# Kernel tuning notes

Measured on AMD Instinct MI355X. Metric: run time of the kernel, lower is better.

## Reference

```python
import jax, jax.numpy as jnp
import numpy as np

N, V, E = 65536, 2048, 1024
TEMPERATURE = 0.5
EPS = 1e-10
LOG_PARAM_Q = -2.995732273553991


def _l2_normalize(x, axis):
    # matches torch F.normalize(p=2): x / max(||x||, 1e-12)
    n = jnp.sqrt(jnp.sum(x * x, axis=axis, keepdims=True))
    return x / jnp.maximum(n, 1e-12)


def setup_inputs() -> dict:
    key = jax.random.key(0)
    k1, k2, k3 = jax.random.split(key, 3)
    z = jax.random.normal(k1, (N, E), dtype=jnp.float32)
    emb_weight = jax.random.normal(k2, (V, E), dtype=jnp.float32)
    U = jax.random.uniform(k3, (N, V), dtype=jnp.float32)
    return {"z": z, "emb_weight": emb_weight, "U": U}


def reference(z, emb_weight, U):
    kappa_q = jnp.exp(jnp.float32(LOG_PARAM_Q)) + jnp.float32(1.0)
    zn = _l2_normalize(z, axis=1)              # [N, E]
    emb = _l2_normalize(emb_weight, axis=1)    # [V, E]
    # logit = -distances = kappa_q * z @ emb.T
    logit = kappa_q * jnp.matmul(zn, emb.T)    # [N, V]
    # gumbel-softmax sample (training branch)
    g = -jnp.log(-jnp.log(U + EPS) + EPS)
    tokens = jax.nn.softmax((logit + g) / TEMPERATURE, axis=-1)  # [N, V]
    z_q = jnp.matmul(tokens, emb)              # [N, E]
    return (tokens, z_q)
```

## Files before the change

kernel.cpp:

```cpp
#include <hip/hip_runtime.h>
#include <hip/hip_bf16.h>
#include <stdint.h>

typedef short bf16x8 __attribute__((ext_vector_type(8)));
typedef float floatx4 __attribute__((ext_vector_type(4)));

#define N_ROWS 65536
#define V_DIM 2048
#define E_DIM 1024

__device__ __forceinline__ short f2bf(float x) {
  union { float f; uint32_t u; } c; c.f = x;
  uint32_t r = (c.u + 0x7FFFu + ((c.u >> 16) & 1u)) >> 16;
  return (short)(uint16_t)r;
}
__device__ __forceinline__ float bf16f(short b) {
  union { uint32_t u; float f; } c; c.u = ((uint32_t)(uint16_t)b) << 16;
  return c.f;
}

__device__ __forceinline__ float wave_sum(float v) {
#pragma unroll
  for (int o = 32; o > 0; o >>= 1) v += __shfl_xor(v, o);
  return v;
}
__device__ __forceinline__ float wave_max(float v) {
#pragma unroll
  for (int o = 32; o > 0; o >>= 1) v = fmaxf(v, __shfl_xor(v, o));
  return v;
}

__device__ __forceinline__ void gll16(const short* g, short* l) {
  __builtin_amdgcn_global_load_lds(
      (const __attribute__((address_space(1))) void*)g,
      (__attribute__((address_space(3))) void*)l, 16, 0, 0);
}

#define FRAG(base, R, c) \
  (*(const bf16x8*)((const char*)(base) + ((R) << 7) + (((((c) >> 3) ^ ((R) & 7))) << 4)))

__global__ __launch_bounds__(256) void k_norm_emb(const float* __restrict__ W,
                                                  short* __restrict__ embn,
                                                  short* __restrict__ embnT) {
  const int v = blockIdx.x;
  const int t = threadIdx.x;
  const int w = t >> 6, l = t & 63;
  const float4 val = *(const float4*)&W[(size_t)v * E_DIM + t * 4];
  float ss = val.x * val.x + val.y * val.y + val.z * val.z + val.w * val.w;
  ss = wave_sum(ss);
  __shared__ float red[4];
  if (l == 0) red[w] = ss;
  __syncthreads();
  ss = red[0] + red[1] + red[2] + red[3];
  const float inv = 1.0f / fmaxf(sqrtf(ss), 1e-12f);
  short4 o;
  o.x = f2bf(val.x * inv);
  o.y = f2bf(val.y * inv);
  o.z = f2bf(val.z * inv);
  o.w = f2bf(val.w * inv);
  *(short4*)&embn[(size_t)v * E_DIM + t * 4] = o;
  embnT[(size_t)(t * 4 + 0) * V_DIM + v] = o.x;
  embnT[(size_t)(t * 4 + 1) * V_DIM + v] = o.y;
  embnT[(size_t)(t * 4 + 2) * V_DIM + v] = o.z;
  embnT[(size_t)(t * 4 + 3) * V_DIM + v] = o.w;
}

__global__ __launch_bounds__(256) void k_norm_z(const float* __restrict__ Z,
                                                short* __restrict__ zn) {
  const int w = threadIdx.x >> 6, l = threadIdx.x & 63;
  const int row = blockIdx.x * 4 + w;
  const float* zr = Z + (size_t)row * E_DIM;
  float4 v[4];
  float ss = 0.f;
#pragma unroll
  for (int i = 0; i < 4; ++i) {
    v[i] = *(const float4*)&zr[(i * 64 + l) * 4];
    ss += v[i].x * v[i].x + v[i].y * v[i].y + v[i].z * v[i].z + v[i].w * v[i].w;
  }
  ss = wave_sum(ss);
  const float SCALE = 2.0f * (expf(-2.995732273553991f) + 1.0f);
  const float inv = SCALE / fmaxf(sqrtf(ss), 1e-12f);
  short* zo = zn + (size_t)row * E_DIM;
#pragma unroll
  for (int i = 0; i < 4; ++i) {
    short4 o;
    o.x = f2bf(v[i].x * inv);
    o.y = f2bf(v[i].y * inv);
    o.z = f2bf(v[i].z * inv);
    o.w = f2bf(v[i].w * inv);
    *(short4*)&zo[(i * 64 + l) * 4] = o;
  }
}

template <int KDIM, int NBX, int EPI>
__global__ __launch_bounds__(512, 2) void k_gemm8(
    const short* __restrict__ A, const short* __restrict__ B,
    const float* __restrict__ U, short* __restrict__ Pb,
    float* __restrict__ partials, const float* __restrict__ invsum,
    float* __restrict__ C, int cpx) {
  __shared__ __align__(16) short Sm[65536];
  const int NT = KDIM / 32;
  const int tid = threadIdx.x;
  const int wv = tid >> 6, lane = tid & 63;
  const int lr = lane & 15, lh = lane >> 4;
  const int wr = wv >> 2, wc = wv & 3;
  const int d = blockIdx.x;
  const int L = (d & 7) * cpx + (d >> 3);
  const int by = L / NBX, bx = L % NBX;
  const int m0 = by * 256, n0 = bx * 256;
  const int sg = (((lane & 3) ^ ((lane >> 2) & 3) ^ ((lane >> 4) & 3)) << 3);
  const int srow = wv * 16 + (lane >> 2);
  const short* gA = A + (size_t)(m0 + srow) * KDIM + sg;
  const short* gB = B + (size_t)(n0 + srow) * KDIM + sg;
  const int fslot = lh ^ ((lr ^ (lr >> 2)) & 3);
  const int aoff = wr * 8192 + lr * 64 + fslot * 16;
  const int boff = wc * 4096 + lr * 64 + fslot * 16;

#pragma unroll
  for (int t = 0; t < 2; ++t) {
#pragma unroll
    for (int q = 0; q < 2; ++q) {
      gll16(gA + (size_t)(q * 128) * KDIM + t * 32, Sm + t * 8192 + q * 4096 + wv * 512);
      gll16(gB + (size_t)(q * 128) * KDIM + t * 32, Sm + 32768 + t * 8192 + q * 4096 + wv * 512);
    }
  }
  asm volatile("s_waitcnt vmcnt(4)" ::: "memory");
  __builtin_amdgcn_s_barrier();
  __builtin_amdgcn_sched_barrier(0);

  floatx4 acc[8][4] = {};

#define DO_TILE(KT, STAGE, VMN)                                                     \
  {                                                                                 \
    const int cb_ = (KT) & 3;                                                       \
    const char* Ab_ = (const char*)Sm + cb_ * 16384;                                \
    const char* Bb_ = (const char*)Sm + 65536 + cb_ * 16384;                        \
    short* An_ = Sm + (((KT) + 2) & 3) * 8192;                                      \
    short* Bn_ = Sm + 32768 + (((KT) + 2) & 3) * 8192;                              \
    const size_t kc_ = (size_t)((KT) + 2) * 32;                                     \
    bf16x8 bfr[4], af[4];                                                           \
     \
    _Pragma("unroll")                                                               \
    for (int n = 0; n < 4; ++n) bfr[n] = *(const bf16x8*)(Bb_ + boff + n * 1024);   \
    _Pragma("unroll")                                                               \
    for (int i = 0; i < 4; ++i) af[i] = *(const bf16x8*)(Ab_ + aoff + i * 1024);    \
    if (STAGE) {                                                                    \
      gll16(gA + kc_, An_ + wv * 512);                                              \
      gll16(gA + (size_t)128 * KDIM + kc_, An_ + 4096 + wv * 512);                  \
    }                                                                               \
    __builtin_amdgcn_s_barrier();                                                   \
    asm volatile("s_waitcnt lgkmcnt(0)" ::: "memory");                              \
    __builtin_amdgcn_sched_barrier(0);                                              \
    __builtin_amdgcn_s_setprio(1);                                                  \
    _Pragma("unroll")                                                               \
    for (int i = 0; i < 4; ++i) {                                                   \
      _Pragma("unroll")                                                             \
      for (int n = 0; n < 4; ++n)                                                   \
        acc[i][n] =                                                                 \
            __builtin_amdgcn_mfma_f32_16x16x32_bf16(af[i], bfr[n], acc[i][n], 0, 0, 0); \
    }                                                                               \
    __builtin_amdgcn_s_setprio(0);                                                  \
    __builtin_amdgcn_s_barrier();                                                   \
     \
    _Pragma("unroll")                                                               \
    for (int i = 0; i < 4; ++i)                                                     \
      af[i] = *(const bf16x8*)(Ab_ + aoff + 4096 + i * 1024);                       \
    if (STAGE) {                                                                    \
      gll16(gB + kc_, Bn_ + wv * 512);                                              \
      gll16(gB + (size_t)128 * KDIM + kc_, Bn_ + 4096 + wv * 512);                  \
    }                                                                               \
    __builtin_amdgcn_s_barrier();                                                   \
    asm volatile("s_waitcnt lgkmcnt(0)" ::: "memory");                              \
    __builtin_amdgcn_sched_barrier(0);                                              \
    __builtin_amdgcn_s_setprio(1);                                                  \
    _Pragma("unroll")                                                               \
    for (int i = 0; i < 4; ++i) {                                                   \
      _Pragma("unroll")                                                             \
      for (int n = 0; n < 4; ++n)                                                   \
        acc[4 + i][n] =                                                             \
            __builtin_amdgcn_mfma_f32_16x16x32_bf16(af[i], bfr[n], acc[4 + i][n], 0, 0, 0); \
    }                                                                               \
    __builtin_amdgcn_s_setprio(0);                                                  \
    asm volatile("s_waitcnt vmcnt(" #VMN ")" ::: "memory");                         \
    __builtin_amdgcn_s_barrier();                                                   \
    __builtin_amdgcn_sched_barrier(0);                                              \
  }

  for (int kt = 0; kt < NT - 2; ++kt) DO_TILE(kt, 1, 4);
  DO_TILE(NT - 2, 0, 0);
  DO_TILE(NT - 1, 0, 0);
#undef DO_TILE

  const int gr0 = m0 + wr * 128 + lh * 4;
  const int gc0 = n0 + wc * 64 + lr;
  if (EPI == 0) {
    float rs[8][4] = {};
#pragma unroll
    for (int m = 0; m < 8; ++m)
#pragma unroll
      for (int n = 0; n < 4; ++n) {
        const int col = gc0 + n * 16;
#pragma unroll
        for (int j = 0; j < 4; ++j) {
          const int row = gr0 + m * 16 + j;
          const size_t idx = (size_t)row * V_DIM + col;
          const float u = U[idx];
          const float e = __expf(acc[m][n][j] - 2.f * __logf(-__logf(u + 1e-10f) + 1e-10f));
          const short eb = f2bf(e);
          Pb[idx] = eb;
          rs[m][j] += bf16f(eb);
        }
      }
#pragma unroll
    for (int m = 0; m < 8; ++m)
#pragma unroll
      for (int j = 0; j < 4; ++j) {
        float s = rs[m][j];
        s += __shfl_xor(s, 1); s += __shfl_xor(s, 2);
        s += __shfl_xor(s, 4); s += __shfl_xor(s, 8);
        if (lr == 0)
          partials[(size_t)(gr0 + m * 16 + j) * 32 + bx * 4 + wc] = s;
      }
  } else {
#pragma unroll
    for (int m = 0; m < 8; ++m)
#pragma unroll
      for (int j = 0; j < 4; ++j) {
        const int row = gr0 + m * 16 + j;
        const float s = invsum[row];
#pragma unroll
        for (int n = 0; n < 4; ++n)
          C[(size_t)row * E_DIM + gc0 + n * 16] = acc[m][n][j] * s;
      }
  }
}

__global__ __launch_bounds__(256) void k_rowsum_inv(const float* __restrict__ partials,
                                                    float* __restrict__ invsum) {
  const int r = blockIdx.x * 256 + threadIdx.x;
  const float4* p = (const float4*)&partials[(size_t)r * 32];
  float s = 0.f;
#pragma unroll
  for (int i = 0; i < 8; ++i) { float4 v = p[i]; s += v.x + v.y + v.z + v.w; }
  invsum[r] = 1.f / s;
}

__global__ __launch_bounds__(256) void k_token_norm(const short* __restrict__ Pb,
                                                    const float* __restrict__ invsum,
                                                    float* __restrict__ tokens) {
  const size_t stride = (size_t)gridDim.x * 256 * 8;
  for (size_t i = ((size_t)blockIdx.x * 256 + threadIdx.x) * 8;
       i < (size_t)N_ROWS * V_DIM; i += stride) {
    const float s = invsum[i >> 11];
    const bf16x8 v = *(const bf16x8*)&Pb[i];
    float4 o0, o1;
    o0.x = bf16f(v[0]) * s; o0.y = bf16f(v[1]) * s;
    o0.z = bf16f(v[2]) * s; o0.w = bf16f(v[3]) * s;
    o1.x = bf16f(v[4]) * s; o1.y = bf16f(v[5]) * s;
    o1.z = bf16f(v[6]) * s; o1.w = bf16f(v[7]) * s;
    *(float4*)&tokens[i] = o0;
    *(float4*)&tokens[i + 4] = o1;
  }
}

__global__ __launch_bounds__(256) void k_gemm_nt(const short* __restrict__ A,
                                                 const short* __restrict__ B,
                                                 float* __restrict__ C,
                                                 int lda, int ldb, int ldc, int K) {
  __shared__ __align__(16) short As[128][64];
  __shared__ __align__(16) short Bs[128][64];
  const int t = threadIdx.x;
  const int w = t >> 6, l = t & 63;
  const int lr = l & 15, lh = l >> 4;
  const int m0 = blockIdx.y * 128, n0 = blockIdx.x * 128;
  const int wm = (w >> 1) * 64, wn = (w & 1) * 64;
  floatx4 acc[4][4] = {};
  for (int k0 = 0; k0 < K; k0 += 64) {
    __syncthreads();
#pragma unroll
    for (int i = 0; i < 4; ++i) {
      const int c = i * 256 + t;
      const int r = c >> 3, c8 = (c & 7) * 8;
      *(bf16x8*)&As[r][c8] = *(const bf16x8*)&A[(size_t)(m0 + r) * lda + k0 + c8];
      *(bf16x8*)&Bs[r][c8] = *(const bf16x8*)&B[(size_t)(n0 + r) * ldb + k0 + c8];
    }
    __syncthreads();
#pragma unroll
    for (int kk = 0; kk < 64; kk += 32) {
      bf16x8 af[4], bfr[4];
#pragma unroll
      for (int m = 0; m < 4; ++m) af[m] = *(const bf16x8*)&As[wm + m * 16 + lr][kk + lh * 8];
#pragma unroll
      for (int n = 0; n < 4; ++n) bfr[n] = *(const bf16x8*)&Bs[wn + n * 16 + lr][kk + lh * 8];
#pragma unroll
      for (int m = 0; m < 4; ++m)
#pragma unroll
        for (int n = 0; n < 4; ++n)
          acc[m][n] = __builtin_amdgcn_mfma_f32_16x16x32_bf16(af[m], bfr[n], acc[m][n], 0, 0, 0);
    }
  }
#pragma unroll
  for (int m = 0; m < 4; ++m)
#pragma unroll
    for (int n = 0; n < 4; ++n) {
      const int col = n0 + wn + n * 16 + lr;
#pragma unroll
      for (int j = 0; j < 4; ++j)
        C[(size_t)(m0 + wm + m * 16 + lh * 4 + j) * ldc + col] = acc[m][n][j];
    }
}

__global__ __launch_bounds__(256) void k_gemm_nt_f32a(const float* __restrict__ A,
                                                      const short* __restrict__ B,
                                                      float* __restrict__ C,
                                                      int lda, int ldb, int ldc, int K) {
  __shared__ __align__(16) short As[128][64];
  __shared__ __align__(16) short Bs[128][64];
  const int t = threadIdx.x;
  const int w = t >> 6, l = t & 63;
  const int lr = l & 15, lh = l >> 4;
  const int m0 = blockIdx.y * 128, n0 = blockIdx.x * 128;
  const int wm = (w >> 1) * 64, wn = (w & 1) * 64;
  floatx4 acc[4][4] = {};
  for (int k0 = 0; k0 < K; k0 += 64) {
    __syncthreads();
#pragma unroll
    for (int i = 0; i < 4; ++i) {
      const int c = i * 256 + t;
      const int r = c >> 3, c8 = (c & 7) * 8;
      const float4 a0 = *(const float4*)&A[(size_t)(m0 + r) * lda + k0 + c8];
      const float4 a1 = *(const float4*)&A[(size_t)(m0 + r) * lda + k0 + c8 + 4];
      bf16x8 va;
      va[0] = f2bf(a0.x); va[1] = f2bf(a0.y); va[2] = f2bf(a0.z); va[3] = f2bf(a0.w);
      va[4] = f2bf(a1.x); va[5] = f2bf(a1.y); va[6] = f2bf(a1.z); va[7] = f2bf(a1.w);
      *(bf16x8*)&As[r][c8] = va;
      *(bf16x8*)&Bs[r][c8] = *(const bf16x8*)&B[(size_t)(n0 + r) * ldb + k0 + c8];
    }
    __syncthreads();
#pragma unroll
    for (int kk = 0; kk < 64; kk += 32) {
      bf16x8 af[4], bfr[4];
#pragma unroll
      for (int m = 0; m < 4; ++m) af[m] = *(const bf16x8*)&As[wm + m * 16 + lr][kk + lh * 8];
#pragma unroll
      for (int n = 0; n < 4; ++n) bfr[n] = *(const bf16x8*)&Bs[wn + n * 16 + lr][kk + lh * 8];
#pragma unroll
      for (int m = 0; m < 4; ++m)
#pragma unroll
        for (int n = 0; n < 4; ++n)
          acc[m][n] = __builtin_amdgcn_mfma_f32_16x16x32_bf16(af[m], bfr[n], acc[m][n], 0, 0, 0);
    }
  }
#pragma unroll
  for (int m = 0; m < 4; ++m)
#pragma unroll
    for (int n = 0; n < 4; ++n) {
      const int col = n0 + wn + n * 16 + lr;
#pragma unroll
      for (int j = 0; j < 4; ++j)
        C[(size_t)(m0 + wm + m * 16 + lh * 4 + j) * ldc + col] = acc[m][n][j];
    }
}

__global__ __launch_bounds__(256) void k_gumbel_softmax(float* __restrict__ S,
                                                        const float* __restrict__ U) {
  const int t = threadIdx.x;
  const int w = t >> 6, l = t & 63;
  const size_t base = (size_t)blockIdx.x * V_DIM + t * 8;
  const float4 s0 = *(const float4*)&S[base];
  const float4 s1 = *(const float4*)&S[base + 4];
  const float4 u0 = *(const float4*)&U[base];
  const float4 u1 = *(const float4*)&U[base + 4];
  float x[8];
  x[0] = s0.x - 2.f * __logf(-__logf(u0.x + 1e-10f) + 1e-10f);
  x[1] = s0.y - 2.f * __logf(-__logf(u0.y + 1e-10f) + 1e-10f);
  x[2] = s0.z - 2.f * __logf(-__logf(u0.z + 1e-10f) + 1e-10f);
  x[3] = s0.w - 2.f * __logf(-__logf(u0.w + 1e-10f) + 1e-10f);
  x[4] = s1.x - 2.f * __logf(-__logf(u1.x + 1e-10f) + 1e-10f);
  x[5] = s1.y - 2.f * __logf(-__logf(u1.y + 1e-10f) + 1e-10f);
  x[6] = s1.z - 2.f * __logf(-__logf(u1.z + 1e-10f) + 1e-10f);
  x[7] = s1.w - 2.f * __logf(-__logf(u1.w + 1e-10f) + 1e-10f);
  float lm = x[0];
#pragma unroll
  for (int i = 1; i < 8; ++i) lm = fmaxf(lm, x[i]);
  lm = wave_max(lm);
  __shared__ float redA[4], redB[4];
  if (l == 0) redA[w] = lm;
  __syncthreads();
  const float m = fmaxf(fmaxf(redA[0], redA[1]), fmaxf(redA[2], redA[3]));
  float p[8];
  float ls = 0.f;
#pragma unroll
  for (int i = 0; i < 8; ++i) { p[i] = __expf(x[i] - m); ls += p[i]; }
  ls = wave_sum(ls);
  if (l == 0) redB[w] = ls;
  __syncthreads();
  const float inv = 1.0f / (redB[0] + redB[1] + redB[2] + redB[3]);
  float4 o0 = make_float4(p[0] * inv, p[1] * inv, p[2] * inv, p[3] * inv);
  float4 o1 = make_float4(p[4] * inv, p[5] * inv, p[6] * inv, p[7] * inv);
  *(float4*)&S[base] = o0;
  *(float4*)&S[base + 4] = o1;
}

extern "C" void kernel_launch(void* const* d_in, const int* in_sizes, int n_in,
                              void* d_out, int out_size, void* d_ws, size_t ws_size,
                              hipStream_t stream) {
  const float* z = (const float*)d_in[0];
  const float* W = (const float*)d_in[1];
  const float* U = (const float*)d_in[2];
  float* tokens = (float*)d_out;
  float* zq = tokens + (size_t)N_ROWS * V_DIM;
  short* zn = (short*)zq;

  short* embn = (short*)d_ws;
  short* embnT = embn + (size_t)V_DIM * E_DIM;

  const size_t NEED = (size_t)V_DIM * E_DIM * 2 * 2
                    + (size_t)N_ROWS * 32 * 4
                    + (size_t)N_ROWS * 4
                    + (size_t)N_ROWS * V_DIM * 2;

  k_norm_emb<<<V_DIM, 256, 0, stream>>>(W, embn, embnT);
  k_norm_z<<<N_ROWS / 4, 256, 0, stream>>>(z, zn);

  if (ws_size >= NEED) {
    float* partials = (float*)(embnT + (size_t)V_DIM * E_DIM);
    float* invsum = partials + (size_t)N_ROWS * 32;
    short* Pb = (short*)(invsum + N_ROWS);
    k_gemm8<E_DIM, 8, 0><<<2048, 512, 0, stream>>>(
        zn, embn, U, Pb, partials, nullptr, nullptr, 2048 / 8);
    k_rowsum_inv<<<N_ROWS / 256, 256, 0, stream>>>(partials, invsum);
    k_token_norm<<<2048, 256, 0, stream>>>(Pb, invsum, tokens);
    k_gemm8<V_DIM, 4, 1><<<1024, 512, 0, stream>>>(
        Pb, embnT, nullptr, nullptr, nullptr, invsum, zq, 1024 / 8);
  } else {
    k_gemm_nt<<<dim3(V_DIM / 128, N_ROWS / 128), 256, 0, stream>>>(
        zn, embn, tokens, E_DIM, E_DIM, V_DIM, E_DIM);
    k_gumbel_softmax<<<N_ROWS, 256, 0, stream>>>(tokens, U);
    k_gemm_nt_f32a<<<dim3(E_DIM / 128, N_ROWS / 128), 256, 0, stream>>>(
        tokens, embnT, zq, V_DIM, V_DIM, E_DIM, V_DIM);
  }
}
```

Measured before the change: 992.7 us.

## Fuse token normalization into second GEMM epilogue and prefetch U in first

Removes the separate token-normalization kernel. Each block of the second GEMM (tokens @ emb) now also re-reads its 256-row by 512-column slice of the bf16 probabilities, scales it by the inverse row sum and writes fp32 tokens. The block mapping of that GEMM changes so adjacent blocks share column tiles, which keeps the Pb rows hot in cache. In the first GEMM the U loads are issued in groups ahead of the exp/log work to hide global latency, at the cost of many more live registers.

```diff
diff --git a/kernel.cpp b/kernel.cpp
--- a/kernel.cpp
+++ b/kernel.cpp
@@ -97,7 +97,7 @@
     const short* __restrict__ A, const short* __restrict__ B,
     const float* __restrict__ U, short* __restrict__ Pb,
     float* __restrict__ partials, const float* __restrict__ invsum,
-    float* __restrict__ C, int cpx) {
+    float* __restrict__ C, float* __restrict__ tokens, int cpx) {
   __shared__ __align__(16) short Sm[65536];
   const int NT = KDIM / 32;
   const int tid = threadIdx.x;
@@ -106,7 +106,8 @@
   const int wr = wv >> 2, wc = wv & 3;
   const int d = blockIdx.x;
   const int L = (d & 7) * cpx + (d >> 3);
-  const int by = L / NBX, bx = L % NBX;
+  const int by = (EPI == 0) ? (L / NBX) : (L & 255);
+  const int bx = (EPI == 0) ? (L % NBX) : (L >> 8);
   const int m0 = by * 256, n0 = bx * 256;
   const int sg = (((lane & 3) ^ ((lane >> 2) & 3) ^ ((lane >> 4) & 3)) << 3);
   const int srow = wv * 16 + (lane >> 2);
@@ -194,23 +195,50 @@
   const int gr0 = m0 + wr * 128 + lh * 4;
   const int gc0 = n0 + wc * 64 + lr;
   if (EPI == 0) {
+    const float* Ug = U + (size_t)gr0 * V_DIM + gc0;
     float rs[8][4] = {};
-#pragma unroll
-    for (int m = 0; m < 8; ++m)
-#pragma unroll
-      for (int n = 0; n < 4; ++n) {
-        const int col = gc0 + n * 16;
-#pragma unroll
-        for (int j = 0; j < 4; ++j) {
-          const int row = gr0 + m * 16 + j;
-          const size_t idx = (size_t)row * V_DIM + col;
-          const float u = U[idx];
-          const float e = __expf(acc[m][n][j] - 2.f * __logf(-__logf(u + 1e-10f) + 1e-10f));
-          const short eb = f2bf(e);
-          Pb[idx] = eb;
-          rs[m][j] += bf16f(eb);
-        }
-      }
+    float u01[32], u23[32], u45[32], u67[32];
+#define UPREF(arr, P)                                                               \
+    {                                                                               \
+      _Pragma("unroll")                                                             \
+      for (int mm = 0; mm < 2; ++mm)                                                \
+        _Pragma("unroll")                                                           \
+        for (int n = 0; n < 4; ++n)                                                 \
+          _Pragma("unroll")                                                         \
+          for (int j = 0; j < 4; ++j)                                               \
+            arr[mm * 16 + n * 4 + j] =                                              \
+                Ug[(size_t)(((2 * (P) + mm) * 16 + j)) * V_DIM + n * 16];           \
+    }
+#define EPI_PAIR(P, arr)                                                            \
+    _Pragma("unroll")                                                               \
+    for (int mm = 0; mm < 2; ++mm) {                                                \
+      const int m = 2 * (P) + mm;                                                   \
+      _Pragma("unroll")                                                             \
+      for (int n = 0; n < 4; ++n) {                                                 \
+        const int col = gc0 + n * 16;                                               \
+        _Pragma("unroll")                                                           \
+        for (int j = 0; j < 4; ++j) {                                               \
+          const int row = gr0 + m * 16 + j;                                         \
+          const size_t idx = (size_t)row * V_DIM + col;                             \
+          const float u = arr[mm * 16 + n * 4 + j];                                 \
+          const float e = __expf(acc[m][n][j] -                                     \
+                                 2.f * __logf(-__logf(u + 1e-10f) + 1e-10f));       \
+          const short eb = f2bf(e);                                                 \
+          Pb[idx] = eb;                                                             \
+          rs[m][j] += bf16f(eb);                                                    \
+        }                                                                           \
+      }                                                                             \
+    }
+    UPREF(u01, 0);
+    UPREF(u23, 1);
+    UPREF(u45, 2);
+    EPI_PAIR(0, u01);
+    UPREF(u67, 3);
+    EPI_PAIR(1, u23);
+    EPI_PAIR(2, u45);
+    EPI_PAIR(3, u67);
+#undef UPREF
+#undef EPI_PAIR
 #pragma unroll
     for (int m = 0; m < 8; ++m)
 #pragma unroll
@@ -232,6 +260,18 @@
         for (int n = 0; n < 4; ++n)
           C[(size_t)row * E_DIM + gc0 + n * 16] = acc[m][n][j] * s;
       }
+    const int tcol0 = bx * 512;
+    const int rowoff = tid >> 7;
+    const int coff = (tid & 127) * 4;
+    for (int it = 0; it < 64; ++it) {
+      const int row = m0 + it * 4 + rowoff;
+      const float s = invsum[row];
+      const short4 pv = *(const short4*)&A[(size_t)row * KDIM + tcol0 + coff];
+      float4 o;
+      o.x = bf16f(pv.x) * s; o.y = bf16f(pv.y) * s;
+      o.z = bf16f(pv.z) * s; o.w = bf16f(pv.w) * s;
+      *(float4*)&tokens[(size_t)row * V_DIM + tcol0 + coff] = o;
+    }
   }
 }
 
@@ -243,24 +283,6 @@
 #pragma unroll
   for (int i = 0; i < 8; ++i) { float4 v = p[i]; s += v.x + v.y + v.z + v.w; }
   invsum[r] = 1.f / s;
-}
-
-__global__ __launch_bounds__(256) void k_token_norm(const short* __restrict__ Pb,
-                                                    const float* __restrict__ invsum,
-                                                    float* __restrict__ tokens) {
-  const size_t stride = (size_t)gridDim.x * 256 * 8;
-  for (size_t i = ((size_t)blockIdx.x * 256 + threadIdx.x) * 8;
-       i < (size_t)N_ROWS * V_DIM; i += stride) {
-    const float s = invsum[i >> 11];
-    const bf16x8 v = *(const bf16x8*)&Pb[i];
-    float4 o0, o1;
-    o0.x = bf16f(v[0]) * s; o0.y = bf16f(v[1]) * s;
-    o0.z = bf16f(v[2]) * s; o0.w = bf16f(v[3]) * s;
-    o1.x = bf16f(v[4]) * s; o1.y = bf16f(v[5]) * s;
-    o1.z = bf16f(v[6]) * s; o1.w = bf16f(v[7]) * s;
-    *(float4*)&tokens[i] = o0;
-    *(float4*)&tokens[i + 4] = o1;
-  }
 }
 
 __global__ __launch_bounds__(256) void k_gemm_nt(const short* __restrict__ A,
@@ -428,11 +450,10 @@
     float* invsum = partials + (size_t)N_ROWS * 32;
     short* Pb = (short*)(invsum + N_ROWS);
     k_gemm8<E_DIM, 8, 0><<<2048, 512, 0, stream>>>(
-        zn, embn, U, Pb, partials, nullptr, nullptr, 2048 / 8);
+        zn, embn, U, Pb, partials, nullptr, nullptr, nullptr, 2048 / 8);
     k_rowsum_inv<<<N_ROWS / 256, 256, 0, stream>>>(partials, invsum);
-    k_token_norm<<<2048, 256, 0, stream>>>(Pb, invsum, tokens);
     k_gemm8<V_DIM, 4, 1><<<1024, 512, 0, stream>>>(
-        Pb, embnT, nullptr, nullptr, nullptr, invsum, zq, 1024 / 8);
+        Pb, embnT, nullptr, nullptr, nullptr, invsum, zq, tokens, 1024 / 8);
   } else {
     k_gemm_nt<<<dim3(V_DIM / 128, N_ROWS / 128), 256, 0, stream>>>(
         zn, embn, tokens, E_DIM, E_DIM, V_DIM, E_DIM);
```

New measurement: 1.039 ms. +4.7%, slower.

## Fuse token normalization into second GEMM epilogue and remap block order

Applied to the files above, without the earlier changes.

Removes the separate token-normalization kernel and has each block of the second GEMM (tokens·emb) write a 256x512 slice of normalized fp32 tokens from the bf16 probabilities after its matmul epilogue. The block-to-tile mapping for that GEMM changes so that consecutive blocks cover different row tiles, and the four column blocks of one row tile together cover all 2048 token columns. This saves a kernel launch and lets the re-read of the bf16 probabilities hit cache lines the GEMM just loaded. In exchange, the 512 MB token write is serialized at the tail of each GEMM block, which lengthens those blocks, and the block reorder may hurt L2 reuse of the embedding matrix.

```diff
diff --git a/kernel.cpp b/kernel.cpp
--- a/kernel.cpp
+++ b/kernel.cpp
@@ -97,7 +97,7 @@
     const short* __restrict__ A, const short* __restrict__ B,
     const float* __restrict__ U, short* __restrict__ Pb,
     float* __restrict__ partials, const float* __restrict__ invsum,
-    float* __restrict__ C, int cpx) {
+    float* __restrict__ C, float* __restrict__ tokens, int cpx) {
   __shared__ __align__(16) short Sm[65536];
   const int NT = KDIM / 32;
   const int tid = threadIdx.x;
@@ -106,7 +106,8 @@
   const int wr = wv >> 2, wc = wv & 3;
   const int d = blockIdx.x;
   const int L = (d & 7) * cpx + (d >> 3);
-  const int by = L / NBX, bx = L % NBX;
+  const int by = (EPI == 0) ? (L / NBX) : (L & 255);
+  const int bx = (EPI == 0) ? (L % NBX) : (L >> 8);
   const int m0 = by * 256, n0 = bx * 256;
   const int sg = (((lane & 3) ^ ((lane >> 2) & 3) ^ ((lane >> 4) & 3)) << 3);
   const int srow = wv * 16 + (lane >> 2);
@@ -232,6 +233,18 @@
         for (int n = 0; n < 4; ++n)
           C[(size_t)row * E_DIM + gc0 + n * 16] = acc[m][n][j] * s;
       }
+    const int tcol0 = bx * 512;
+    const int rowoff = tid >> 7;
+    const int coff = (tid & 127) * 4;
+    for (int it = 0; it < 64; ++it) {
+      const int row = m0 + it * 4 + rowoff;
+      const float s = invsum[row];
+      const short4 pv = *(const short4*)&A[(size_t)row * KDIM + tcol0 + coff];
+      float4 o;
+      o.x = bf16f(pv.x) * s; o.y = bf16f(pv.y) * s;
+      o.z = bf16f(pv.z) * s; o.w = bf16f(pv.w) * s;
+      *(float4*)&tokens[(size_t)row * V_DIM + tcol0 + coff] = o;
+    }
   }
 }
 
@@ -243,24 +256,6 @@
 #pragma unroll
   for (int i = 0; i < 8; ++i) { float4 v = p[i]; s += v.x + v.y + v.z + v.w; }
   invsum[r] = 1.f / s;
-}
-
-__global__ __launch_bounds__(256) void k_token_norm(const short* __restrict__ Pb,
-                                                    const float* __restrict__ invsum,
-                                                    float* __restrict__ tokens) {
-  const size_t stride = (size_t)gridDim.x * 256 * 8;
-  for (size_t i = ((size_t)blockIdx.x * 256 + threadIdx.x) * 8;
-       i < (size_t)N_ROWS * V_DIM; i += stride) {
-    const float s = invsum[i >> 11];
-    const bf16x8 v = *(const bf16x8*)&Pb[i];
-    float4 o0, o1;
-    o0.x = bf16f(v[0]) * s; o0.y = bf16f(v[1]) * s;
-    o0.z = bf16f(v[2]) * s; o0.w = bf16f(v[3]) * s;
-    o1.x = bf16f(v[4]) * s; o1.y = bf16f(v[5]) * s;
-    o1.z = bf16f(v[6]) * s; o1.w = bf16f(v[7]) * s;
-    *(float4*)&tokens[i] = o0;
-    *(float4*)&tokens[i + 4] = o1;
-  }
 }
 
 __global__ __launch_bounds__(256) void k_gemm_nt(const short* __restrict__ A,
@@ -428,11 +423,10 @@
     float* invsum = partials + (size_t)N_ROWS * 32;
     short* Pb = (short*)(invsum + N_ROWS);
     k_gemm8<E_DIM, 8, 0><<<2048, 512, 0, stream>>>(
-        zn, embn, U, Pb, partials, nullptr, nullptr, 2048 / 8);
+        zn, embn, U, Pb, partials, nullptr, nullptr, nullptr, 2048 / 8);
     k_rowsum_inv<<<N_ROWS / 256, 256, 0, stream>>>(partials, invsum);
-    k_token_norm<<<2048, 256, 0, stream>>>(Pb, invsum, tokens);
     k_gemm8<V_DIM, 4, 1><<<1024, 512, 0, stream>>>(
-        Pb, embnT, nullptr, nullptr, nullptr, invsum, zq, 1024 / 8);
+        Pb, embnT, nullptr, nullptr, nullptr, invsum, zq, tokens, 1024 / 8);
   } else {
     k_gemm_nt<<<dim3(V_DIM / 128, N_ROWS / 128), 256, 0, stream>>>(
         zn, embn, tokens, E_DIM, E_DIM, V_DIM, E_DIM);
```

After: 1.033 ms. +4.1%, slower.
